# Performance work log

Hardware: AMD Instinct MI355X
Metric: run time of the kernel (lower is better)

Reference implementation:

```python
import jax, jax.numpy as jnp
import numpy as np
import math

B, S, D, H = 2, 2048, 2048, 16
DH = D // H  # head dim = 128
THETA = 10000.0


def _rope(x, pos):
    """Interleaved RoPE. x: [..., S, DH], pos: [S] (int)."""
    dh = x.shape[-1]
    freqs = (1.0 / THETA) ** (2.0 * jnp.arange(dh // 2, dtype=jnp.float32) / dh)  # [DH/2]
    ang = pos.astype(jnp.float32)[:, None] * freqs[None, :]  # [S, DH/2]
    cos = jnp.cos(ang).astype(x.dtype)
    sin = jnp.sin(ang).astype(x.dtype)
    xe = x[..., 0::2]
    xo = x[..., 1::2]
    oe = xe * cos - xo * sin
    oo = xe * sin + xo * cos
    return jnp.stack([oe, oo], axis=-1).reshape(x.shape)


def setup_inputs() -> dict:
    key = jax.random.key(0)
    ks = jax.random.split(key, 5)
    std = 2.0 / math.sqrt(D + D)
    x = jax.random.normal(ks[0], (B, S, D), dtype=jnp.float32)
    Wq = jax.random.normal(ks[1], (D, D), dtype=jnp.float32) * std
    Wk = jax.random.normal(ks[2], (D, D), dtype=jnp.float32) * std
    Wv = jax.random.normal(ks[3], (D, D), dtype=jnp.float32) * std
    Wo = jax.random.normal(ks[4], (D, D), dtype=jnp.float32) * std
    token_positions = jnp.arange(S, dtype=jnp.int64 if jax.config.jax_enable_x64 else jnp.int32)[None, :]
    return {"x": x, "token_positions": token_positions, "Wq": Wq, "Wk": Wk, "Wv": Wv, "Wo": Wo}


def reference(x, token_positions, Wq, Wk, Wv, Wo):
    b, s, d = x.shape
    pos = token_positions[0]  # [S]
    # QKV projections (Linear is x @ W.T, no bias)
    Q = (x @ Wq.T).reshape(b, s, H, DH).transpose(0, 2, 1, 3)  # [b,h,s,dh]
    K = (x @ Wk.T).reshape(b, s, H, DH).transpose(0, 2, 1, 3)
    V = (x @ Wv.T).reshape(b, s, H, DH).transpose(0, 2, 1, 3)
    # per-head RoPE on Q and K
    Q = _rope(Q, pos)
    K = _rope(K, pos)
    # scaled dot-product attention with causal mask
    scores = jnp.einsum('bhqd,bhkd->bhqk', Q, K) / math.sqrt(DH)
    causal = jnp.tril(jnp.ones((s, s), dtype=bool))  # [s,s]
    scores = jnp.where(causal[None, None, :, :], scores, -jnp.inf)
    prob = jax.nn.softmax(scores, axis=-1)
    O = jnp.einsum('bhqk,bhkd->bhqd', prob, V)  # [b,h,s,dh]
    O = O.transpose(0, 2, 1, 3).reshape(b, s, d)
    return O @ Wo.T
```

## Files before the change

kernel.cpp:

```cpp
#include <hip/hip_runtime.h>
#include <hip/hip_bf16.h>
#include <math.h>

#define BB 2
#define SS 2048
#define DD 2048
#define HH 16
#define DHH 128
#define MM (BB*SS)

typedef __attribute__((ext_vector_type(8))) short bf16x8;
typedef __attribute__((ext_vector_type(4))) float f32x4;

#define AS1 __attribute__((address_space(1)))
#define AS3 __attribute__((address_space(3)))
#define GLOAD_LDS16(g, l) __builtin_amdgcn_global_load_lds((const AS1 void*)(g), (AS3 void*)(l), 16, 0, 0)

#if __has_builtin(__builtin_amdgcn_exp2f)
#define EXP2F(x) __builtin_amdgcn_exp2f(x)
#else
#define EXP2F(x) exp2f(x)
#endif

__device__ __forceinline__ float b2f(short s) {
  union { unsigned int u; float f; } v;
  v.u = ((unsigned int)(unsigned short)s) << 16;
  return v.f;
}
__device__ __forceinline__ short f2b(float f) {
  union { float f; unsigned int u; } v; v.f = f;
  unsigned int u = v.u;
  u += 0x7fffu + ((u >> 16) & 1u);
  return (short)(u >> 16);
}
__device__ __forceinline__ short f2b_fast(float f) {
  union { float f; unsigned int u; } v; v.f = f;
  return (short)((v.u + 0x8000u) >> 16);
}

template<int CTRL>
__device__ __forceinline__ float dppf(float x) {
  int xi = __builtin_bit_cast(int, x);
  int r = __builtin_amdgcn_update_dpp(0, xi, CTRL, 0xf, 0xf, true);
  return __builtin_bit_cast(float, r);
}
__device__ __forceinline__ float rmax16(float x) {
  x = fmaxf(x, dppf<0xB1>(x));
  x = fmaxf(x, dppf<0x4E>(x));
  x = fmaxf(x, dppf<0x141>(x));
  x = fmaxf(x, dppf<0x140>(x));
  return x;
}
__device__ __forceinline__ float rsum16(float x) {
  x += dppf<0xB1>(x);
  x += dppf<0x4E>(x);
  x += dppf<0x141>(x);
  x += dppf<0x140>(x);
  return x;
}

__global__ void cvt_all(const float* __restrict__ x,  const float* __restrict__ wq,
                        const float* __restrict__ wk, const float* __restrict__ wv,
                        const float* __restrict__ wo,
                        short* __restrict__ xb,  short* __restrict__ wqb,
                        short* __restrict__ wkb, short* __restrict__ wvb,
                        short* __restrict__ wob) {
  int i = blockIdx.x * blockDim.x + threadIdx.x;
  const float* src; short* dst; int off;
  if (i < 2097152) { src = x; dst = xb; off = i; }
  else {
    int j = i - 2097152;
    int w = j >> 20; off = j & 1048575;
    src = (w == 0) ? wq : (w == 1) ? wk : (w == 2) ? wv : wo;
    dst = (w == 0) ? wqb : (w == 1) ? wkb : (w == 2) ? wvb : wob;
  }
  float4 v = ((const float4*)src)[i < 2097152 ? off : off];
  short4 o;
  o.x = f2b(v.x); o.y = f2b(v.y); o.z = f2b(v.z); o.w = f2b(v.w);
  ((short4*)dst)[off] = o;
}

__global__ __launch_bounds__(256, 2)
void gemm_qkv(const short* __restrict__ A,
              const short* __restrict__ Wq, const short* __restrict__ Wk,
              const short* __restrict__ Wv, const int* __restrict__ pos,
              short* __restrict__ Qo, short* __restrict__ Ko, short* __restrict__ Vo) {
  __shared__ __align__(16) short As[256*64];
  __shared__ __align__(16) short Bs[128*64];
  const int tid = threadIdx.x;
  const int lane = tid & 63;
  const int wave = tid >> 6;
  const int quad = lane >> 4, l16 = lane & 15;
  const int wsel = blockIdx.x >> 4;
  const short* Bw = Wq; short* Cout = Qo;
  if (wsel == 1) { Bw = Wk; Cout = Ko; }
  else if (wsel == 2) { Bw = Wv; Cout = Vo; }
  const int bn = (blockIdx.x & 15) * 128;
  const int bm = blockIdx.y * 256;
  const int K = DD;

  const int srow = tid >> 3;
  const int scol = (tid & 7) * 8;
  const short* aBase = A + (size_t)(bm + srow) * K + scol;
  const short* bBase = Bw + (size_t)(bn + srow) * K + scol;
  f32x4 acc[4][8] = {};

  for (int k0 = 0; k0 < K; k0 += 64) {
    #pragma unroll
    for (int j = 0; j < 8; ++j)
      GLOAD_LDS16(aBase + (size_t)j * 32 * K + k0, As + j * 2048 + wave * 512);
    #pragma unroll
    for (int j = 0; j < 4; ++j)
      GLOAD_LDS16(bBase + (size_t)j * 32 * K + k0, Bs + j * 2048 + wave * 512);
    __syncthreads();
    #pragma unroll
    for (int kk = 0; kk < 64; kk += 32) {
      bf16x8 af[4], bf[8];
      #pragma unroll
      for (int t = 0; t < 4; ++t)
        af[t] = *(const bf16x8*)&As[(wave*64 + t*16 + l16) * 64 + kk + quad*8];
      #pragma unroll
      for (int t = 0; t < 8; ++t)
        bf[t] = *(const bf16x8*)&Bs[(t*16 + l16) * 64 + kk + quad*8];
      #pragma unroll
      for (int mt = 0; mt < 4; ++mt)
        #pragma unroll
        for (int nt = 0; nt < 8; ++nt)
          acc[mt][nt] = __builtin_amdgcn_mfma_f32_16x16x32_bf16(af[mt], bf[nt], acc[mt][nt], 0, 0, 0);
    }
    __syncthreads();
  }

  if (wsel < 2) {
    const float post = (wsel == 0) ? 0.1275174306f : 1.0f;
    float fr[8];
    #pragma unroll
    for (int nt = 0; nt < 8; ++nt) {
      int pi = nt*8 + (l16 >> 1);
      fr[nt] = __expf(-0.14391156831f * (float)pi);
    }
    const float sgn = (l16 & 1) ? 1.0f : -1.0f;
    #pragma unroll
    for (int mt = 0; mt < 4; ++mt) {
      #pragma unroll
      for (int r = 0; r < 4; ++r) {
        int m = bm + wave*64 + mt*16 + quad*4 + r;
        float fp = (float)pos[m & 2047];
        #pragma unroll
        for (int nt = 0; nt < 8; ++nt) {
          float v = acc[mt][nt][r];
          float p = dppf<0xB1>(v);
          float ang = fp * fr[nt];
          float sn = __sinf(ang), cs = __cosf(ang);
          acc[mt][nt][r] = (v * cs + sgn * p * sn) * post;
        }
      }
    }
  }

  #pragma unroll
  for (int mt = 0; mt < 4; ++mt)
    #pragma unroll
    for (int nt = 0; nt < 8; ++nt)
      #pragma unroll
      for (int r = 0; r < 4; ++r) {
        int m = bm + wave*64 + mt*16 + quad*4 + r;
        int n = bn + nt*16 + l16;
        int b = m >> 11, s = m & 2047;
        int h = n >> 7,  d = n & 127;
        Cout[(((size_t)(b*HH + h)*SS + s)*DHH) + d] = f2b(acc[mt][nt][r]);
      }
}

__global__ __launch_bounds__(256)
void gemm_o(const short* __restrict__ A, const short* __restrict__ Bw,
            float* __restrict__ Cout) {
  __shared__ __align__(16) short As[128*64];
  __shared__ __align__(16) short Bs[128*64];
  const int tid = threadIdx.x;
  const int lane = tid & 63;
  const int wave = tid >> 6;
  const int wm = wave >> 1, wn = wave & 1;
  const int quad = lane >> 4, l16 = lane & 15;
  const int bm = blockIdx.y * 128, bn = blockIdx.x * 128;
  const int K = DD;

  const int srow = tid >> 3;
  const int scol = (tid & 7) * 8;
  const short* aBase = A + (size_t)(bm + srow) * K + scol;
  const short* bBase = Bw + (size_t)(bn + srow) * K + scol;
  f32x4 acc[4][4] = {};

  for (int k0 = 0; k0 < K; k0 += 64) {
    #pragma unroll
    for (int j = 0; j < 4; ++j) {
      GLOAD_LDS16(aBase + (size_t)j * 32 * K + k0, As + j * 2048 + wave * 512);
      GLOAD_LDS16(bBase + (size_t)j * 32 * K + k0, Bs + j * 2048 + wave * 512);
    }
    __syncthreads();
    #pragma unroll
    for (int kk = 0; kk < 64; kk += 32) {
      bf16x8 af[4], bf[4];
      #pragma unroll
      for (int t = 0; t < 4; ++t)
        af[t] = *(const bf16x8*)&As[(wm*64 + t*16 + l16) * 64 + kk + quad*8];
      #pragma unroll
      for (int t = 0; t < 4; ++t)
        bf[t] = *(const bf16x8*)&Bs[(wn*64 + t*16 + l16) * 64 + kk + quad*8];
      #pragma unroll
      for (int mt = 0; mt < 4; ++mt)
        #pragma unroll
        for (int nt = 0; nt < 4; ++nt)
          acc[mt][nt] = __builtin_amdgcn_mfma_f32_16x16x32_bf16(af[mt], bf[nt], acc[mt][nt], 0, 0, 0);
    }
    __syncthreads();
  }

  #pragma unroll
  for (int mt = 0; mt < 4; ++mt)
    #pragma unroll
    for (int nt = 0; nt < 4; ++nt)
      #pragma unroll
      for (int r = 0; r < 4; ++r) {
        int m = bm + wm*64 + mt*16 + quad*4 + r;
        int n = bn + wn*64 + nt*16 + l16;
        Cout[(size_t)m * DD + n] = acc[mt][nt][r];
      }
}

__global__ __launch_bounds__(512, 4)
void attn(const short* __restrict__ Q, const short* __restrict__ K,
          const short* __restrict__ V, short* __restrict__ O) {
  __shared__ __align__(16) short Ks[64*128];
  __shared__ __align__(16) short Vt[128*64];
  __shared__ __align__(16) short Pb[8*16*64];
  const int tid = threadIdx.x;
  const int lane = tid & 63, wave = tid >> 6;
  const int quad = lane >> 4, l16 = lane & 15;
  const int p = blockIdx.x;
  const int qa = p, qb = 31 - p;
  const int bh = blockIdx.y;
  const int b = bh >> 4, h = bh & 15;
  const short* Kg = K + (size_t)bh * SS * DHH;
  const short* Vg = V + (size_t)bh * SS * DHH;

  const int wt = wave >> 2;
  const int qtile = wt ? qb : qa;
  const int qbase = qtile * 64 + (wave & 3) * 16;

  bf16x8 aq[4];
  {
    const short* qp = Q + ((size_t)bh * SS + qbase + l16) * DHH + quad*8;
    #pragma unroll
    for (int ks = 0; ks < 4; ++ks) aq[ks] = *(const bf16x8*)(qp + ks*32);
  }

  f32x4 o[8] = {};
  float mrow[4], lrow[4];
  #pragma unroll
  for (int r = 0; r < 4; ++r) { mrow[r] = -1e30f; lrow[r] = 0.f; }

  const int krow = tid >> 3;
  const int kcolb = (tid & 7) * 32;
  const int vkp = (tid & 31) * 2;
  const int vds = (tid >> 5) * 8;

  const int nkt = qb + 1;
  int4 kreg[2], vreg[2];
  {
    const short* kp = Kg + (size_t)krow * DHH + (kcolb >> 1);
    kreg[0] = *(const int4*)kp; kreg[1] = *(const int4*)(kp + 8);
    const short* vp = Vg + (size_t)vkp * DHH + vds;
    vreg[0] = *(const int4*)vp; vreg[1] = *(const int4*)(vp + DHH);
  }

  for (int kt = 0; kt < nkt; ++kt) {
    #pragma unroll
    for (int j = 0; j < 2; ++j)
      *(int4*)((char*)Ks + krow*256 + ((kcolb + j*16) ^ ((krow & 7) << 4))) = kreg[j];
    {
      const short* s0 = (const short*)&vreg[0];
      const short* s1 = (const short*)&vreg[1];
      #pragma unroll
      for (int e = 0; e < 8; ++e) {
        int dim = vds + e;
        int val = (int)(unsigned short)s0[e] | ((int)(unsigned short)s1[e] << 16);
        *(int*)((char*)Vt + dim*128 + ((vkp*2) ^ ((dim & 7) << 4))) = val;
      }
    }
    __syncthreads();

    if (kt + 1 < nkt) {
      const short* kp = Kg + (size_t)((kt+1)*64 + krow) * DHH + (kcolb >> 1);
      kreg[0] = *(const int4*)kp; kreg[1] = *(const int4*)(kp + 8);
      const short* vp = Vg + (size_t)((kt+1)*64 + vkp) * DHH + vds;
      vreg[0] = *(const int4*)vp; vreg[1] = *(const int4*)(vp + DHH);
    }

    if (kt <= qtile) {
      float sv[4][4];
      __builtin_amdgcn_s_setprio(1);
      #pragma unroll
      for (int nt = 0; nt < 4; ++nt) {
        f32x4 a = {0.f, 0.f, 0.f, 0.f};
        #pragma unroll
        for (int ks = 0; ks < 4; ++ks) {
          int key = nt*16 + l16;
          bf16x8 bk = *(const bf16x8*)((const char*)Ks + key*256 +
                         ((ks*64 + quad*16) ^ ((key & 7) << 4)));
          a = __builtin_amdgcn_mfma_f32_16x16x32_bf16(aq[ks], bk, a, 0, 0, 0);
        }
        #pragma unroll
        for (int r = 0; r < 4; ++r) sv[nt][r] = a[r];
      }
      __builtin_amdgcn_s_setprio(0);

      if (kt == qtile) {
        #pragma unroll
        for (int nt = 0; nt < 4; ++nt)
          #pragma unroll
          for (int r = 0; r < 4; ++r)
            if (nt*16 + l16 > (wave & 3)*16 + quad*4 + r) sv[nt][r] = -1e30f;
      }

      #pragma unroll
      for (int r = 0; r < 4; ++r) {
        float mx = fmaxf(fmaxf(sv[0][r], sv[1][r]), fmaxf(sv[2][r], sv[3][r]));
        mx = rmax16(mx);
        float mnew = fmaxf(mrow[r], mx);
        float alpha = EXP2F(mrow[r] - mnew);
        float ls = 0.f;
        #pragma unroll
        for (int nt = 0; nt < 4; ++nt) {
          float pv = EXP2F(sv[nt][r] - mnew);
          sv[nt][r] = pv; ls += pv;
        }
        ls = rsum16(ls);
        lrow[r] = lrow[r] * alpha + ls;
        mrow[r] = mnew;
        #pragma unroll
        for (int nt = 0; nt < 8; ++nt) o[nt][r] *= alpha;
      }

      #pragma unroll
      for (int nt = 0; nt < 4; ++nt)
        #pragma unroll
        for (int r = 0; r < 4; ++r) {
          int qr = quad*4 + r;
          *(short*)((char*)Pb + wave*2048 + qr*128 +
                    (((nt*16 + l16)*2) ^ ((qr & 7) << 4))) = f2b_fast(sv[nt][r]);
        }

      bf16x8 ap[2];
      #pragma unroll
      for (int k2 = 0; k2 < 2; ++k2)
        ap[k2] = *(const bf16x8*)((const char*)Pb + wave*2048 + l16*128 +
                    ((k2*64 + quad*16) ^ ((l16 & 7) << 4)));

      __builtin_amdgcn_s_setprio(1);
      #pragma unroll
      for (int k2 = 0; k2 < 2; ++k2)
        #pragma unroll
        for (int nt = 0; nt < 8; ++nt) {
          int d = nt*16 + l16;
          bf16x8 bv = *(const bf16x8*)((const char*)Vt + d*128 +
                         ((k2*64 + quad*16) ^ ((d & 7) << 4)));
          o[nt] = __builtin_amdgcn_mfma_f32_16x16x32_bf16(ap[k2], bv, o[nt], 0, 0, 0);
        }
      __builtin_amdgcn_s_setprio(0);
    }
    __syncthreads();
  }

  #pragma unroll
  for (int nt = 0; nt < 8; ++nt)
    #pragma unroll
    for (int r = 0; r < 4; ++r) {
      int q = qbase + quad*4 + r;
      float v = o[nt][r] / lrow[r];
      O[((size_t)(b*SS + q)) * DD + h*DHH + nt*16 + l16] = f2b(v);
    }
}

extern "C" void kernel_launch(void* const* d_in, const int* in_sizes, int n_in,
                              void* d_out, int out_size, void* d_ws, size_t ws_size,
                              hipStream_t stream) {
  const float* x  = (const float*)d_in[0];
  const int* pos  = (const int*)d_in[1];
  const float* Wq = (const float*)d_in[2];
  const float* Wk = (const float*)d_in[3];
  const float* Wv = (const float*)d_in[4];
  const float* Wo = (const float*)d_in[5];

  char* ws = (char*)d_ws;
  short* xb  = (short*)(ws);
  short* wqb = (short*)(ws + 16777216);
  short* wkb = (short*)(ws + 25165824);
  short* wvb = (short*)(ws + 33554432);
  short* wob = (short*)(ws + 41943040);
  short* Qb  = (short*)(ws + 50331648);
  short* Kb  = (short*)(ws + 67108864);
  short* Vb  = (short*)(ws + 83886080);
  short* Ob  = (short*)(ws + 100663296);

  cvt_all<<<24576, 256, 0, stream>>>(x, Wq, Wk, Wv, Wo, xb, wqb, wkb, wvb, wob);

  dim3 gq(48, MM/256);
  gemm_qkv<<<gq, 256, 0, stream>>>(xb, wqb, wkb, wvb, pos, Qb, Kb, Vb);

  dim3 ga(16, BB*HH);
  attn<<<ga, 512, 0, stream>>>(Qb, Kb, Vb, Ob);

  dim3 go(DD/128, MM/128);
  gemm_o<<<go, 256, 0, stream>>>(Ob, wob, (float*)d_out);
}
```

Baseline: 443.6 us.

## Rewrite QKV GEMM as 256x256 double-buffered, swizzled, 8-wave pipelined kernel

The QKV projection GEMM moves from a 256x128 tile with 4 waves and a single LDS buffer to a 256x256 tile with 8 waves (2x4 wave grid). It double-buffers LDS, uses an XOR swizzle to avoid bank conflicts, and interleaves the next tile's global->LDS loads with MFMA quadrants under fine-grained barriers and s_setprio. The goal is to hide global load latency and raise arithmetic intensity per block. In exchange it uses 128KB of LDS, gets more register pressure, and launches half as many blocks, which may lower occupancy.

```diff
diff --git a/kernel.cpp b/kernel.cpp
--- a/kernel.cpp
+++ b/kernel.cpp
@@ -80,74 +80,119 @@
   ((short4*)dst)[off] = o;
 }
 
-__global__ __launch_bounds__(256, 2)
+#define LDA(cb, mt, kk) (*(const bf16x8*)((const char*)smA + (cb)*32768 + \
+    (wm*128 + (mt)*16 + l16)*128 + (((kk)*64 + quad*16) ^ ((l16 & 7) << 4))))
+#define LDB(cb, nt, kk) (*(const bf16x8*)((const char*)smB + (cb)*32768 + \
+    (wn*64 + (nt)*16 + l16)*128 + (((kk)*64 + quad*16) ^ ((l16 & 7) << 4))))
+#define STGA(b, t, h) do { \
+    GLOAD_LDS16(aBase + (size_t)((h)*128) * DD + (t)*64,      smA + (b)*16384 + ((h)*128)*64 + wst); \
+    GLOAD_LDS16(aBase + (size_t)((h)*128 + 64) * DD + (t)*64, smA + (b)*16384 + ((h)*128 + 64)*64 + wst); } while(0)
+#define STGB(b, t, h) do { \
+    GLOAD_LDS16(bBase + (size_t)((h)*128) * DD + (t)*64,      smB + (b)*16384 + ((h)*128)*64 + wst); \
+    GLOAD_LDS16(bBase + (size_t)((h)*128 + 64) * DD + (t)*64, smB + (b)*16384 + ((h)*128 + 64)*64 + wst); } while(0)
+#define MFMA_Q(MT0, NT0) do { \
+    __builtin_amdgcn_s_setprio(1); \
+    _Pragma("unroll") \
+    for (int mt = 0; mt < 4; ++mt) \
+      _Pragma("unroll") \
+      for (int nt = 0; nt < 2; ++nt) \
+        _Pragma("unroll") \
+        for (int kk = 0; kk < 2; ++kk) \
+          acc[(MT0) + mt][(NT0) + nt] = __builtin_amdgcn_mfma_f32_16x16x32_bf16( \
+              af[mt][kk], bf[(NT0) + nt][kk], acc[(MT0) + mt][(NT0) + nt], 0, 0, 0); \
+    __builtin_amdgcn_s_setprio(0); } while(0)
+
+__global__ __launch_bounds__(512, 2)
 void gemm_qkv(const short* __restrict__ A,
               const short* __restrict__ Wq, const short* __restrict__ Wk,
               const short* __restrict__ Wv, const int* __restrict__ pos,
               short* __restrict__ Qo, short* __restrict__ Ko, short* __restrict__ Vo) {
-  __shared__ __align__(16) short As[256*64];
-  __shared__ __align__(16) short Bs[128*64];
+  __shared__ __align__(16) short sm[65536];
   const int tid = threadIdx.x;
   const int lane = tid & 63;
   const int wave = tid >> 6;
   const int quad = lane >> 4, l16 = lane & 15;
-  const int wsel = blockIdx.x >> 4;
-  const short* Bw = Wq; short* Cout = Qo;
-  if (wsel == 1) { Bw = Wk; Cout = Ko; }
-  else if (wsel == 2) { Bw = Wv; Cout = Vo; }
-  const int bn = (blockIdx.x & 15) * 128;
+  const int wm = wave >> 2, wn = wave & 3;
+  const int wsel = blockIdx.x >> 3;
+  const short* Bw = (wsel == 0) ? Wq : (wsel == 1) ? Wk : Wv;
+  short* Cout = (wsel == 0) ? Qo : (wsel == 1) ? Ko : Vo;
+  const int bn = (blockIdx.x & 7) * 256;
   const int bm = blockIdx.y * 256;
-  const int K = DD;
+
+  short* smA = sm;
+  short* smB = sm + 32768;
+  const int wst = wave * 512;
 
   const int srow = tid >> 3;
-  const int scol = (tid & 7) * 8;
-  const short* aBase = A + (size_t)(bm + srow) * K + scol;
-  const short* bBase = Bw + (size_t)(bn + srow) * K + scol;
-  f32x4 acc[4][8] = {};
-
-  for (int k0 = 0; k0 < K; k0 += 64) {
-    #pragma unroll
-    for (int j = 0; j < 8; ++j)
-      GLOAD_LDS16(aBase + (size_t)j * 32 * K + k0, As + j * 2048 + wave * 512);
-    #pragma unroll
-    for (int j = 0; j < 4; ++j)
-      GLOAD_LDS16(bBase + (size_t)j * 32 * K + k0, Bs + j * 2048 + wave * 512);
-    __syncthreads();
-    #pragma unroll
-    for (int kk = 0; kk < 64; kk += 32) {
-      bf16x8 af[4], bf[8];
-      #pragma unroll
-      for (int t = 0; t < 4; ++t)
-        af[t] = *(const bf16x8*)&As[(wave*64 + t*16 + l16) * 64 + kk + quad*8];
-      #pragma unroll
-      for (int t = 0; t < 8; ++t)
-        bf[t] = *(const bf16x8*)&Bs[(t*16 + l16) * 64 + kk + quad*8];
-      #pragma unroll
-      for (int mt = 0; mt < 4; ++mt)
-        #pragma unroll
-        for (int nt = 0; nt < 8; ++nt)
-          acc[mt][nt] = __builtin_amdgcn_mfma_f32_16x16x32_bf16(af[mt], bf[nt], acc[mt][nt], 0, 0, 0);
-    }
-    __syncthreads();
+  const int scol = ((tid & 7) ^ (srow & 7)) * 8;
+  const short* aBase = A  + (size_t)(bm + srow) * DD + scol;
+  const short* bBase = Bw + (size_t)(bn + srow) * DD + scol;
+
+  f32x4 acc[8][4] = {};
+  bf16x8 af[4][2], bf[4][2];
+
+  STGA(0, 0, 0); STGA(0, 0, 1);
+  STGB(0, 0, 0); STGB(0, 0, 1);
+  STGB(1, 1, 0); STGB(1, 1, 1);
+  asm volatile("s_waitcnt vmcnt(4)" ::: "memory");
+  __builtin_amdgcn_s_barrier();
+
+  for (int t = 0; t < 32; ++t) {
+    const int cb = t & 1, nb = cb ^ 1;
+    #pragma unroll
+    for (int mt = 0; mt < 4; ++mt) { af[mt][0] = LDA(cb, mt, 0); af[mt][1] = LDA(cb, mt, 1); }
+    #pragma unroll
+    for (int nt = 0; nt < 2; ++nt) { bf[nt][0] = LDB(cb, nt, 0); bf[nt][1] = LDB(cb, nt, 1); }
+    if (t + 1 < 32) STGA(nb, t + 1, 0);
+    __builtin_amdgcn_s_barrier();
+    asm volatile("s_waitcnt lgkmcnt(0)" ::: "memory");
+    __builtin_amdgcn_sched_barrier(0);
+    MFMA_Q(0, 0);
+    __builtin_amdgcn_s_barrier();
+    #pragma unroll
+    for (int nt = 2; nt < 4; ++nt) { bf[nt][0] = LDB(cb, nt, 0); bf[nt][1] = LDB(cb, nt, 1); }
+    if (t + 1 < 32) STGA(nb, t + 1, 1);
+    __builtin_amdgcn_s_barrier();
+    asm volatile("s_waitcnt lgkmcnt(0)" ::: "memory");
+    __builtin_amdgcn_sched_barrier(0);
+    MFMA_Q(0, 2);
+    __builtin_amdgcn_s_barrier();
+    #pragma unroll
+    for (int mt = 0; mt < 4; ++mt) { af[mt][0] = LDA(cb, mt + 4, 0); af[mt][1] = LDA(cb, mt + 4, 1); }
+    if (t + 2 < 32) STGB(cb, t + 2, 0);
+    __builtin_amdgcn_s_barrier();
+    asm volatile("s_waitcnt lgkmcnt(0)" ::: "memory");
+    __builtin_amdgcn_sched_barrier(0);
+    MFMA_Q(4, 2);
+    __builtin_amdgcn_s_barrier();
+    if (t + 2 < 32) {
+      STGB(cb, t + 2, 1);
+      asm volatile("s_waitcnt vmcnt(4)" ::: "memory");
+    } else {
+      asm volatile("s_waitcnt vmcnt(0)" ::: "memory");
+    }
+    __builtin_amdgcn_s_barrier();
+    MFMA_Q(4, 0);
+    __builtin_amdgcn_s_barrier();
   }
 
   if (wsel < 2) {
     const float post = (wsel == 0) ? 0.1275174306f : 1.0f;
-    float fr[8];
-    #pragma unroll
-    for (int nt = 0; nt < 8; ++nt) {
-      int pi = nt*8 + (l16 >> 1);
+    float fr[4];
+    #pragma unroll
+    for (int nt = 0; nt < 4; ++nt) {
+      int pi = (wn & 1) * 32 + nt * 8 + (l16 >> 1);
       fr[nt] = __expf(-0.14391156831f * (float)pi);
     }
     const float sgn = (l16 & 1) ? 1.0f : -1.0f;
     #pragma unroll
-    for (int mt = 0; mt < 4; ++mt) {
+    for (int mt = 0; mt < 8; ++mt) {
       #pragma unroll
       for (int r = 0; r < 4; ++r) {
-        int m = bm + wave*64 + mt*16 + quad*4 + r;
+        int m = bm + wm*128 + mt*16 + quad*4 + r;
         float fp = (float)pos[m & 2047];
         #pragma unroll
-        for (int nt = 0; nt < 8; ++nt) {
+        for (int nt = 0; nt < 4; ++nt) {
           float v = acc[mt][nt][r];
           float p = dppf<0xB1>(v);
           float ang = fp * fr[nt];
@@ -159,13 +204,13 @@
   }
 
   #pragma unroll
-  for (int mt = 0; mt < 4; ++mt)
-    #pragma unroll
-    for (int nt = 0; nt < 8; ++nt)
+  for (int mt = 0; mt < 8; ++mt)
+    #pragma unroll
+    for (int nt = 0; nt < 4; ++nt)
       #pragma unroll
       for (int r = 0; r < 4; ++r) {
-        int m = bm + wave*64 + mt*16 + quad*4 + r;
-        int n = bn + nt*16 + l16;
+        int m = bm + wm*128 + mt*16 + quad*4 + r;
+        int n = bn + wn*64 + nt*16 + l16;
         int b = m >> 11, s = m & 2047;
         int h = n >> 7,  d = n & 127;
         Cout[(((size_t)(b*HH + h)*SS + s)*DHH) + d] = f2b(acc[mt][nt][r]);
@@ -405,8 +450,8 @@
 
   cvt_all<<<24576, 256, 0, stream>>>(x, Wq, Wk, Wv, Wo, xb, wqb, wkb, wvb, wob);
 
-  dim3 gq(48, MM/256);
-  gemm_qkv<<<gq, 256, 0, stream>>>(xb, wqb, wkb, wvb, pos, Qb, Kb, Vb);
+  dim3 gq(24, MM/256);
+  gemm_qkv<<<gq, 512, 0, stream>>>(xb, wqb, wkb, wvb, pos, Qb, Kb, Vb);
 
   dim3 ga(16, BB*HH);
   attn<<<ga, 512, 0, stream>>>(Qb, Kb, Vb, Ob);
```

Result: faster. 427.0 us (-3.7%).
